# Optimization experiments

Hardware: AMD Instinct MI355X
Metric: run time of the kernel (lower is better)

Reference implementation:

```python
import jax, jax.numpy as jnp
import numpy as np

N_HEADS = 16
D_HEAD = 64
D_MODEL = 1024
N_CTX = 2048
ATTN_SCALE = float(np.sqrt(D_HEAD))
NEG_INF = -jnp.inf


def setup_inputs() -> dict:
    key = jax.random.key(0)
    ks = jax.random.split(key, 6)
    B, S = 2, N_CTX
    q = jax.random.normal(ks[0], (B, S, N_HEADS * D_HEAD), dtype=jnp.float32)
    k = jax.random.normal(ks[1], (B, S, N_HEADS * D_HEAD), dtype=jnp.float32)
    v = jax.random.normal(ks[2], (B, S, N_HEADS * D_HEAD), dtype=jnp.float32)
    residual = jax.random.normal(ks[3], (B, S, D_MODEL), dtype=jnp.float32)
    W_O = jax.random.normal(ks[4], (N_HEADS, D_HEAD, D_MODEL), dtype=jnp.float32) * 0.02
    b_O = jnp.zeros((D_MODEL,), dtype=jnp.float32)
    return {"q": q, "k": k, "v": v, "residual": residual, "W_O": W_O, "b_O": b_O}


def reference(q, k, v, residual, W_O, b_O):
    B, S, _ = q.shape
    # split heads: [..., pos, (h d)] -> [..., pos, h, d]
    qh = q.reshape(B, S, N_HEADS, D_HEAD)
    kh = k.reshape(B, S, N_HEADS, D_HEAD)
    vh = v.reshape(B, S, N_HEADS, D_HEAD)
    # attention scores: [b, h, q_pos, k_pos]
    scores = jnp.einsum('bqhd,bkhd->bhqk', qh, kh) / ATTN_SCALE
    causal = jnp.tril(jnp.ones((S, S), dtype=bool))
    scores = jnp.where(causal, scores, NEG_INF)
    pattern = jax.nn.softmax(scores, axis=-1)
    # z: [b, q_pos, h, d]
    z = jnp.einsum('bkhd,bhqk->bqhd', vh, pattern)
    out = jnp.einsum('bqhd,hdm->bqm', z, W_O) + b_O
    return out, residual
```

## Files before the change

kernel.cpp:

```cpp
#include <hip/hip_runtime.h>

#define BATCH 2
#define SEQ 2048
#define NHEADS 16
#define DHEAD 64
#define DMODEL 1024

typedef __attribute__((ext_vector_type(8))) short bf16x8;
typedef __attribute__((ext_vector_type(4))) float f32x4;

#define QSCALE 0.18033688011112042f

__device__ __forceinline__ unsigned short f2b(float f) {
  union { float f; unsigned u; } a; a.f = f;
  return (unsigned short)((a.u + 0x7fffu + ((a.u >> 16) & 1u)) >> 16);
}

__device__ __forceinline__ unsigned cvt2(float lo, float hi) {
  unsigned r;
  asm("v_cvt_pk_bf16_f32 %0, %1, %2" : "=v"(r) : "v"(lo), "v"(hi));
  return r;
}

#if defined(__has_builtin)
#if __has_builtin(__builtin_amdgcn_exp2f)
#define EXP2(x) __builtin_amdgcn_exp2f(x)
#else
#define EXP2(x) exp2f(x)
#endif
#else
#define EXP2(x) exp2f(x)
#endif

__global__ __launch_bounds__(256) void prep_kernel(
    const float* __restrict__ qg, const float* __restrict__ kg,
    const float* __restrict__ vg, const float* __restrict__ wo,
    const float* __restrict__ residual,
    unsigned short* __restrict__ qb, unsigned short* __restrict__ kb,
    unsigned short* __restrict__ vt, unsigned short* __restrict__ wt,
    float* __restrict__ res_out) {
  __shared__ unsigned short T[64][72];
  const int blk = blockIdx.x;
  const int tid = (int)threadIdx.x;

  if (blk < 4096) {
    const int t = blk * 256 + tid;
    const int d8 = t & 7;
    const int h = (t >> 3) & 15;
    const int q = (t >> 7) & 2047;
    const int b = (t >> 18) & 1;
    const int tensor = (t >> 19) & 1;
    const float* src = (tensor ? kg : qg) +
        ((size_t)(b * SEQ + q) * DMODEL + h * DHEAD + d8 * 8);
    unsigned short* dst = (tensor ? kb : qb) +
        ((size_t)((b * NHEADS + h) * SEQ + q) * DHEAD + d8 * 8);
    const float s = tensor ? 1.0f : QSCALE;
    f32x4 v0 = *(const f32x4*)src;
    f32x4 v1 = *(const f32x4*)(src + 4);
    ushort4 o0, o1;
    o0.x = f2b(v0[0] * s); o0.y = f2b(v0[1] * s);
    o0.z = f2b(v0[2] * s); o0.w = f2b(v0[3] * s);
    o1.x = f2b(v1[0] * s); o1.y = f2b(v1[1] * s);
    o1.z = f2b(v1[2] * s); o1.w = f2b(v1[3] * s);
    *(ushort4*)dst = o0;
    *(ushort4*)(dst + 4) = o1;
  } else if (blk < 5120) {
    const size_t i = ((size_t)(blk - 4096) * 256 + tid) * 16;
    #pragma unroll
    for (int j = 0; j < 4; ++j)
      *(f32x4*)(res_out + i + j * 4) = *(const f32x4*)(residual + i + j * 4);
  } else if (blk < 6144) {
    const int wg = blk - 5120;
    const int kt = wg & 31;
    const int bh = wg >> 5;
    const int row = tid >> 2, quad = tid & 3;
    const int b = bh >> 4, h = bh & 15;
    const float* vp = vg + (size_t)(b * SEQ + kt * 64 + row) * DMODEL + h * DHEAD + quad * 16;
    #pragma unroll
    for (int j = 0; j < 4; ++j) {
      f32x4 x = *(const f32x4*)(vp + j * 4);
      ushort4 o;
      o.x = f2b(x[0]); o.y = f2b(x[1]); o.z = f2b(x[2]); o.w = f2b(x[3]);
      *(ushort4*)&T[row][quad * 16 + j * 4] = o;
    }
    __syncthreads();
    unsigned short* op = vt + ((size_t)bh * DHEAD + row) * SEQ + kt * 64 + quad * 16;
    bf16x8 a, c;
    #pragma unroll
    for (int e = 0; e < 8; ++e) a[e] = (short)T[quad * 16 + e][row];
    #pragma unroll
    for (int e = 0; e < 8; ++e) c[e] = (short)T[quad * 16 + 8 + e][row];
    *(bf16x8*)op = a;
    *(bf16x8*)(op + 8) = c;
  } else {
    const int wg = blk - 6144;
    const int mt = wg & 15;
    const int h = wg >> 4;
    const int row = tid >> 2, quad = tid & 3;
    const float* wp = wo + (size_t)(h * DHEAD + row) * DMODEL + mt * 64 + quad * 16;
    #pragma unroll
    for (int j = 0; j < 4; ++j) {
      f32x4 x = *(const f32x4*)(wp + j * 4);
      ushort4 o;
      o.x = f2b(x[0]); o.y = f2b(x[1]); o.z = f2b(x[2]); o.w = f2b(x[3]);
      *(ushort4*)&T[row][quad * 16 + j * 4] = o;
    }
    __syncthreads();
    unsigned short* op = wt + (size_t)(mt * 64 + row) * DMODEL + h * DHEAD + quad * 16;
    bf16x8 a, c;
    #pragma unroll
    for (int e = 0; e < 8; ++e) a[e] = (short)T[quad * 16 + e][row];
    #pragma unroll
    for (int e = 0; e < 8; ++e) c[e] = (short)T[quad * 16 + 8 + e][row];
    *(bf16x8*)op = a;
    *(bf16x8*)(op + 8) = c;
  }
}

__global__ __launch_bounds__(256) void attn_kernel(
    const unsigned short* __restrict__ qb, const unsigned short* __restrict__ kb,
    const unsigned short* __restrict__ vt, unsigned short* __restrict__ zg) {
  __shared__ unsigned short Kld[64][72];
  __shared__ unsigned short Vtld[64][72];
  __shared__ unsigned short Pld[4][16][72];

  const int wg = (blockIdx.x & 7) * 128 + (blockIdx.x >> 3);
  const int bh = wg >> 5;
  const int qt = (wg & 31) ^ (bh & 31);
  const int tid = (int)threadIdx.x;
  const int w = tid >> 6;
  const int lane = tid & 63;
  const int lg = lane >> 4;
  const int ln = lane & 15;

  bf16x8 qf[2];
  {
    const unsigned short* qp =
        qb + ((size_t)bh * SEQ + qt * 64 + w * 16 + ln) * DHEAD;
    qf[0] = *(const bf16x8*)(qp + lg * 8);
    qf[1] = *(const bf16x8*)(qp + 32 + lg * 8);
  }

  float mrow = -1e30f, lrow = 0.f;
  f32x4 zac[4];
  #pragma unroll
  for (int u = 0; u < 4; ++u) {
    zac[u][0] = 0.f; zac[u][1] = 0.f; zac[u][2] = 0.f; zac[u][3] = 0.f;
  }

  const int row = tid >> 2, quad = tid & 3;
  const int nkt = qt + 1;
  for (int kt = 0; kt < nkt; ++kt) {
    const int k0 = kt * 64;
    {
      const unsigned short* kp = kb + ((size_t)bh * SEQ + k0 + row) * DHEAD + quad * 16;
      const unsigned short* vp = vt + ((size_t)bh * DHEAD + row) * SEQ + k0 + quad * 16;
      *(bf16x8*)&Kld[row][quad * 16]      = *(const bf16x8*)kp;
      *(bf16x8*)&Kld[row][quad * 16 + 8]  = *(const bf16x8*)(kp + 8);
      *(bf16x8*)&Vtld[row][quad * 16]     = *(const bf16x8*)vp;
      *(bf16x8*)&Vtld[row][quad * 16 + 8] = *(const bf16x8*)(vp + 8);
    }
    __syncthreads();

    f32x4 sc[4];
    #pragma unroll
    for (int t = 0; t < 4; ++t) {
      f32x4 s = {0.f, 0.f, 0.f, 0.f};
      #pragma unroll
      for (int c = 0; c < 2; ++c) {
        bf16x8 kf = *(const bf16x8*)&Kld[t * 16 + ln][c * 32 + lg * 8];
        s = __builtin_amdgcn_mfma_f32_16x16x32_bf16(kf, qf[c], s, 0, 0, 0);
      }
      sc[t] = s;
    }

    if (kt == qt) {
      const int qloc = w * 16 + ln;
      #pragma unroll
      for (int t = 0; t < 4; ++t) {
        #pragma unroll
        for (int r = 0; r < 4; ++r) {
          if (t * 16 + lg * 4 + r > qloc) sc[t][r] = -1e30f;
        }
      }
    }

    float mx = sc[0][0];
    #pragma unroll
    for (int t = 0; t < 4; ++t) {
      #pragma unroll
      for (int r = 0; r < 4; ++r) mx = fmaxf(mx, sc[t][r]);
    }
    mx = fmaxf(mx, __shfl_xor(mx, 16, 64));
    mx = fmaxf(mx, __shfl_xor(mx, 32, 64));

    if (!__all(mx <= mrow + 8.f)) {
      const float mnew = fmaxf(mrow, mx);
      const float scl = EXP2(mrow - mnew);
      mrow = mnew;
      lrow *= scl;
      const int sbase = lane & 48;
      const float s0 = __shfl(scl, sbase | (lg * 4 + 0), 64);
      const float s1 = __shfl(scl, sbase | (lg * 4 + 1), 64);
      const float s2 = __shfl(scl, sbase | (lg * 4 + 2), 64);
      const float s3 = __shfl(scl, sbase | (lg * 4 + 3), 64);
      #pragma unroll
      for (int u = 0; u < 4; ++u) {
        zac[u][0] *= s0; zac[u][1] *= s1; zac[u][2] *= s2; zac[u][3] *= s3;
      }
    }

    float rsum = 0.f;
    #pragma unroll
    for (int t = 0; t < 4; ++t) {
      const float p0 = EXP2(sc[t][0] - mrow);
      const float p1 = EXP2(sc[t][1] - mrow);
      const float p2 = EXP2(sc[t][2] - mrow);
      const float p3 = EXP2(sc[t][3] - mrow);
      rsum += (p0 + p1) + (p2 + p3);
      uint2 pk;
      pk.x = cvt2(p0, p1);
      pk.y = cvt2(p2, p3);
      *(uint2*)&Pld[w][ln][t * 16 + lg * 4] = pk;
    }
    rsum += __shfl_xor(rsum, 16, 64);
    rsum += __shfl_xor(rsum, 32, 64);
    lrow += rsum;

    #pragma unroll
    for (int c = 0; c < 2; ++c) {
      bf16x8 pa = *(const bf16x8*)&Pld[w][ln][c * 32 + lg * 8];
      #pragma unroll
      for (int u = 0; u < 4; ++u) {
        bf16x8 vb = *(const bf16x8*)&Vtld[u * 16 + ln][c * 32 + lg * 8];
        zac[u] = __builtin_amdgcn_mfma_f32_16x16x32_bf16(pa, vb, zac[u], 0, 0, 0);
      }
    }
    __syncthreads();
  }

  const int b = bh >> 4, h = bh & 15;
  const int sbase = lane & 48;
  float rl[4];
  #pragma unroll
  for (int i = 0; i < 4; ++i)
    rl[i] = 1.0f / __shfl(lrow, sbase | (lg * 4 + i), 64);
  #pragma unroll
  for (int u = 0; u < 4; ++u) {
    #pragma unroll
    for (int i = 0; i < 4; ++i) {
      const int qrow = qt * 64 + w * 16 + lg * 4 + i;
      zg[((size_t)(b * SEQ + qrow)) * DMODEL + h * DHEAD + u * 16 + ln] =
          f2b(zac[u][i] * rl[i]);
    }
  }
}

__global__ __launch_bounds__(256) void proj_kernel(
    const unsigned short* __restrict__ zb, const unsigned short* __restrict__ wt,
    const float* __restrict__ bo, float* __restrict__ out) {
  __shared__ unsigned short Ald[128][72];
  __shared__ unsigned short Bld[64][72];

  const int m0 = blockIdx.x * 128, n0 = blockIdx.y * 64;
  const int tid = (int)threadIdx.x;
  const int w = tid >> 6, lane = tid & 63, lg = lane >> 4, ln = lane & 15;
  const int wr = w >> 1, wc = w & 1;

  const int arow = tid >> 1, acol = (tid & 1) * 32;
  const int brow = tid >> 2, bcol = (tid & 3) * 16;

  f32x4 acc[4][2];
  #pragma unroll
  for (int a = 0; a < 4; ++a)
    #pragma unroll
    for (int bj = 0; bj < 2; ++bj) {
      acc[a][bj][0] = 0.f; acc[a][bj][1] = 0.f;
      acc[a][bj][2] = 0.f; acc[a][bj][3] = 0.f;
    }

  bf16x8 ra[4], rb[2];
  {
    const unsigned short* ap = zb + (size_t)(m0 + arow) * DMODEL + acol;
    const unsigned short* bp = wt + (size_t)(n0 + brow) * DMODEL + bcol;
    #pragma unroll
    for (int j = 0; j < 4; ++j) ra[j] = *(const bf16x8*)(ap + j * 8);
    rb[0] = *(const bf16x8*)(bp);
    rb[1] = *(const bf16x8*)(bp + 8);
  }

  for (int ks = 0; ks < DMODEL / 64; ++ks) {
    __syncthreads();
    #pragma unroll
    for (int j = 0; j < 4; ++j) *(bf16x8*)&Ald[arow][acol + j * 8] = ra[j];
    *(bf16x8*)&Bld[brow][bcol]     = rb[0];
    *(bf16x8*)&Bld[brow][bcol + 8] = rb[1];
    __syncthreads();

    if (ks + 1 < DMODEL / 64) {
      const int k0 = (ks + 1) * 64;
      const unsigned short* ap = zb + (size_t)(m0 + arow) * DMODEL + k0 + acol;
      const unsigned short* bp = wt + (size_t)(n0 + brow) * DMODEL + k0 + bcol;
      #pragma unroll
      for (int j = 0; j < 4; ++j) ra[j] = *(const bf16x8*)(ap + j * 8);
      rb[0] = *(const bf16x8*)(bp);
      rb[1] = *(const bf16x8*)(bp + 8);
    }

    #pragma unroll
    for (int c = 0; c < 2; ++c) {
      bf16x8 bf[2];
      #pragma unroll
      for (int bj = 0; bj < 2; ++bj)
        bf[bj] = *(const bf16x8*)&Bld[wc * 32 + bj * 16 + ln][c * 32 + lg * 8];
      #pragma unroll
      for (int a = 0; a < 4; ++a) {
        bf16x8 af = *(const bf16x8*)&Ald[wr * 64 + a * 16 + ln][c * 32 + lg * 8];
        #pragma unroll
        for (int bj = 0; bj < 2; ++bj)
          acc[a][bj] = __builtin_amdgcn_mfma_f32_16x16x32_bf16(af, bf[bj], acc[a][bj], 0, 0, 0);
      }
    }
  }

  #pragma unroll
  for (int a = 0; a < 4; ++a)
    #pragma unroll
    for (int bj = 0; bj < 2; ++bj) {
      const int nc = n0 + wc * 32 + bj * 16 + ln;
      const float bias = bo[nc];
      #pragma unroll
      for (int i = 0; i < 4; ++i) {
        const int mr = m0 + wr * 64 + a * 16 + lg * 4 + i;
        out[(size_t)mr * DMODEL + nc] = acc[a][bj][i] + bias;
      }
    }
}

extern "C" void kernel_launch(void* const* d_in, const int* in_sizes, int n_in,
                              void* d_out, int out_size, void* d_ws, size_t ws_size,
                              hipStream_t stream) {
  const float* q        = (const float*)d_in[0];
  const float* k        = (const float*)d_in[1];
  const float* v        = (const float*)d_in[2];
  const float* residual = (const float*)d_in[3];
  const float* wo       = (const float*)d_in[4];
  const float* bo       = (const float*)d_in[5];
  float* out = (float*)d_out;

  const size_t QN = (size_t)BATCH * NHEADS * SEQ * DHEAD;
  unsigned short* qbuf = (unsigned short*)d_ws;
  unsigned short* kbuf = qbuf + QN;
  unsigned short* vtb  = qbuf + 2 * QN;
  unsigned short* wtb  = qbuf + 3 * QN;
  unsigned short* zb   = qbuf + 3 * QN + (size_t)DMODEL * DMODEL;

  prep_kernel<<<dim3(6400), 256, 0, stream>>>(
      q, k, v, wo, residual, qbuf, kbuf, vtb, wtb,
      out + (size_t)BATCH * SEQ * DMODEL);
  attn_kernel<<<dim3(BATCH * NHEADS * (SEQ / 64)), 256, 0, stream>>>(qbuf, kbuf, vtb, zb);
  proj_kernel<<<dim3(BATCH * SEQ / 128, DMODEL / 64), 256, 0, stream>>>(zb, wtb, bo, out);
}
```

Measured before the change: 202.1 us.

## Pair complementary causal q-tiles per block, prefetch K/V, deepen proj K-step

Each attention workgroup now handles two query tiles (ip and 31-ip), so every block does the same amount of causal work and shares each staged K/V tile between both. The grid is halved. The next K/V tile is prefetched into registers while the current one is computed, and the LDS padding changes from 72 to 68. The projection GEMM now stages 128-wide K slices, which halves its barrier count but raises register and LDS use. The exp2 builtin is replaced with exp2f, and the 68-column padding risks misaligned 16-byte LDS accesses and bank conflicts.

```diff
diff --git a/kernel.cpp b/kernel.cpp
--- a/kernel.cpp
+++ b/kernel.cpp
@@ -22,15 +22,7 @@
   return r;
 }
 
-#if defined(__has_builtin)
-#if __has_builtin(__builtin_amdgcn_exp2f)
-#define EXP2(x) __builtin_amdgcn_exp2f(x)
-#else
 #define EXP2(x) exp2f(x)
-#endif
-#else
-#define EXP2(x) exp2f(x)
-#endif
 
 __global__ __launch_bounds__(256) void prep_kernel(
     const float* __restrict__ qg, const float* __restrict__ kg,
@@ -120,48 +112,46 @@
 __global__ __launch_bounds__(256) void attn_kernel(
     const unsigned short* __restrict__ qb, const unsigned short* __restrict__ kb,
     const unsigned short* __restrict__ vt, unsigned short* __restrict__ zg) {
-  __shared__ unsigned short Kld[64][72];
-  __shared__ unsigned short Vtld[64][72];
-  __shared__ unsigned short Pld[4][16][72];
-
-  const int wg = (blockIdx.x & 7) * 128 + (blockIdx.x >> 3);
-  const int bh = wg >> 5;
-  const int qt = (wg & 31) ^ (bh & 31);
+  __shared__ unsigned short Kld[64][68];
+  __shared__ unsigned short Vtld[64][68];
+  __shared__ unsigned short Pld[4][16][68];
+
+  const int wg = (blockIdx.x & 7) * 64 + (blockIdx.x >> 3);
+  const int bh = wg >> 4;
+  const int ip = wg & 15;
+  const int qtA = ip, qtB = 31 - ip;
   const int tid = (int)threadIdx.x;
   const int w = tid >> 6;
   const int lane = tid & 63;
   const int lg = lane >> 4;
   const int ln = lane & 15;
 
-  bf16x8 qf[2];
+  bf16x8 qfA[2], qfB[2];
   {
-    const unsigned short* qp =
-        qb + ((size_t)bh * SEQ + qt * 64 + w * 16 + ln) * DHEAD;
-    qf[0] = *(const bf16x8*)(qp + lg * 8);
-    qf[1] = *(const bf16x8*)(qp + 32 + lg * 8);
-  }
-
-  float mrow = -1e30f, lrow = 0.f;
-  f32x4 zac[4];
+    const unsigned short* qpA =
+        qb + ((size_t)bh * SEQ + qtA * 64 + w * 16 + ln) * DHEAD;
+    const unsigned short* qpB =
+        qb + ((size_t)bh * SEQ + qtB * 64 + w * 16 + ln) * DHEAD;
+    qfA[0] = *(const bf16x8*)(qpA + lg * 8);
+    qfA[1] = *(const bf16x8*)(qpA + 32 + lg * 8);
+    qfB[0] = *(const bf16x8*)(qpB + lg * 8);
+    qfB[1] = *(const bf16x8*)(qpB + 32 + lg * 8);
+  }
+
+  float mA = -1e30f, lA = 0.f, mB = -1e30f, lB = 0.f;
+  f32x4 zacA[4], zacB[4];
   #pragma unroll
   for (int u = 0; u < 4; ++u) {
-    zac[u][0] = 0.f; zac[u][1] = 0.f; zac[u][2] = 0.f; zac[u][3] = 0.f;
+    zacA[u][0] = 0.f; zacA[u][1] = 0.f; zacA[u][2] = 0.f; zacA[u][3] = 0.f;
+    zacB[u][0] = 0.f; zacB[u][1] = 0.f; zacB[u][2] = 0.f; zacB[u][3] = 0.f;
   }
 
   const int row = tid >> 2, quad = tid & 3;
-  const int nkt = qt + 1;
-  for (int kt = 0; kt < nkt; ++kt) {
-    const int k0 = kt * 64;
-    {
-      const unsigned short* kp = kb + ((size_t)bh * SEQ + k0 + row) * DHEAD + quad * 16;
-      const unsigned short* vp = vt + ((size_t)bh * DHEAD + row) * SEQ + k0 + quad * 16;
-      *(bf16x8*)&Kld[row][quad * 16]      = *(const bf16x8*)kp;
-      *(bf16x8*)&Kld[row][quad * 16 + 8]  = *(const bf16x8*)(kp + 8);
-      *(bf16x8*)&Vtld[row][quad * 16]     = *(const bf16x8*)vp;
-      *(bf16x8*)&Vtld[row][quad * 16 + 8] = *(const bf16x8*)(vp + 8);
-    }
-    __syncthreads();
-
+  const unsigned short* kbase = kb + (size_t)bh * SEQ * DHEAD;
+  const unsigned short* vbase = vt + (size_t)bh * DHEAD * SEQ;
+
+  auto compute = [&](const bf16x8* qf, float& mrow, float& lrow, f32x4* zac,
+                     bool diag) {
     f32x4 sc[4];
     #pragma unroll
     for (int t = 0; t < 4; ++t) {
@@ -173,24 +163,19 @@
       }
       sc[t] = s;
     }
-
-    if (kt == qt) {
+    if (diag) {
       const int qloc = w * 16 + ln;
       #pragma unroll
-      for (int t = 0; t < 4; ++t) {
+      for (int t = 0; t < 4; ++t)
         #pragma unroll
-        for (int r = 0; r < 4; ++r) {
+        for (int r = 0; r < 4; ++r)
           if (t * 16 + lg * 4 + r > qloc) sc[t][r] = -1e30f;
-        }
-      }
-    }
-
+    }
     float mx = sc[0][0];
     #pragma unroll
-    for (int t = 0; t < 4; ++t) {
+    for (int t = 0; t < 4; ++t)
       #pragma unroll
       for (int r = 0; r < 4; ++r) mx = fmaxf(mx, sc[t][r]);
-    }
     mx = fmaxf(mx, __shfl_xor(mx, 16, 64));
     mx = fmaxf(mx, __shfl_xor(mx, 32, 64));
 
@@ -236,39 +221,68 @@
         zac[u] = __builtin_amdgcn_mfma_f32_16x16x32_bf16(pa, vb, zac[u], 0, 0, 0);
       }
     }
+  };
+
+  const int nkt = qtB + 1;
+  bf16x8 rk0, rk1, rv0, rv1;
+  {
+    const unsigned short* kp = kbase + (size_t)row * DHEAD + quad * 16;
+    const unsigned short* vp = vbase + (size_t)row * SEQ + quad * 16;
+    rk0 = *(const bf16x8*)kp;  rk1 = *(const bf16x8*)(kp + 8);
+    rv0 = *(const bf16x8*)vp;  rv1 = *(const bf16x8*)(vp + 8);
+  }
+
+  for (int kt = 0; kt < nkt; ++kt) {
+    if (kt) __syncthreads();
+    *(bf16x8*)&Kld[row][quad * 16]      = rk0;
+    *(bf16x8*)&Kld[row][quad * 16 + 8]  = rk1;
+    *(bf16x8*)&Vtld[row][quad * 16]     = rv0;
+    *(bf16x8*)&Vtld[row][quad * 16 + 8] = rv1;
     __syncthreads();
+    if (kt + 1 < nkt) {
+      const int k0 = (kt + 1) * 64;
+      const unsigned short* kp = kbase + (size_t)(k0 + row) * DHEAD + quad * 16;
+      const unsigned short* vp = vbase + (size_t)row * SEQ + k0 + quad * 16;
+      rk0 = *(const bf16x8*)kp;  rk1 = *(const bf16x8*)(kp + 8);
+      rv0 = *(const bf16x8*)vp;  rv1 = *(const bf16x8*)(vp + 8);
+    }
+    if (kt <= qtA) compute(qfA, mA, lA, zacA, kt == qtA);
+    compute(qfB, mB, lB, zacB, kt == qtB);
   }
 
   const int b = bh >> 4, h = bh & 15;
   const int sbase = lane & 48;
-  float rl[4];
-  #pragma unroll
-  for (int i = 0; i < 4; ++i)
-    rl[i] = 1.0f / __shfl(lrow, sbase | (lg * 4 + i), 64);
-  #pragma unroll
-  for (int u = 0; u < 4; ++u) {
-    #pragma unroll
-    for (int i = 0; i < 4; ++i) {
-      const int qrow = qt * 64 + w * 16 + lg * 4 + i;
-      zg[((size_t)(b * SEQ + qrow)) * DMODEL + h * DHEAD + u * 16 + ln] =
-          f2b(zac[u][i] * rl[i]);
-    }
-  }
+  auto epi = [&](int qt, float lrow, const f32x4* zac) {
+    float rl[4];
+    #pragma unroll
+    for (int i = 0; i < 4; ++i)
+      rl[i] = 1.0f / __shfl(lrow, sbase | (lg * 4 + i), 64);
+    #pragma unroll
+    for (int u = 0; u < 4; ++u)
+      #pragma unroll
+      for (int i = 0; i < 4; ++i) {
+        const int qrow = qt * 64 + w * 16 + lg * 4 + i;
+        zg[((size_t)(b * SEQ + qrow)) * DMODEL + h * DHEAD + u * 16 + ln] =
+            f2b(zac[u][i] * rl[i]);
+      }
+  };
+  epi(qtA, lA, zacA);
+  epi(qtB, lB, zacB);
 }
 
 __global__ __launch_bounds__(256) void proj_kernel(
     const unsigned short* __restrict__ zb, const unsigned short* __restrict__ wt,
     const float* __restrict__ bo, float* __restrict__ out) {
-  __shared__ unsigned short Ald[128][72];
-  __shared__ unsigned short Bld[64][72];
+  __shared__ unsigned short Ald[128][136];
+  __shared__ unsigned short Bld[64][136];
 
   const int m0 = blockIdx.x * 128, n0 = blockIdx.y * 64;
   const int tid = (int)threadIdx.x;
   const int w = tid >> 6, lane = tid & 63, lg = lane >> 4, ln = lane & 15;
   const int wr = w >> 1, wc = w & 1;
 
-  const int arow = tid >> 1, acol = (tid & 1) * 32;
-  const int brow = tid >> 2, bcol = (tid & 3) * 16;
+  const int arow = tid >> 1, acol = (tid & 1) * 64;
+  const int brow = tid >> 2, bcol = (tid & 3) * 32;
 
   f32x4 acc[4][2];
   #pragma unroll
@@ -279,36 +293,36 @@
       acc[a][bj][2] = 0.f; acc[a][bj][3] = 0.f;
     }
 
-  bf16x8 ra[4], rb[2];
+  bf16x8 ra[8], rb[4];
   {
     const unsigned short* ap = zb + (size_t)(m0 + arow) * DMODEL + acol;
     const unsigned short* bp = wt + (size_t)(n0 + brow) * DMODEL + bcol;
     #pragma unroll
-    for (int j = 0; j < 4; ++j) ra[j] = *(const bf16x8*)(ap + j * 8);
-    rb[0] = *(const bf16x8*)(bp);
-    rb[1] = *(const bf16x8*)(bp + 8);
-  }
-
-  for (int ks = 0; ks < DMODEL / 64; ++ks) {
+    for (int j = 0; j < 8; ++j) ra[j] = *(const bf16x8*)(ap + j * 8);
+    #pragma unroll
+    for (int j = 0; j < 4; ++j) rb[j] = *(const bf16x8*)(bp + j * 8);
+  }
+
+  for (int ks = 0; ks < DMODEL / 128; ++ks) {
+    if (ks) __syncthreads();
+    #pragma unroll
+    for (int j = 0; j < 8; ++j) *(bf16x8*)&Ald[arow][acol + j * 8] = ra[j];
+    #pragma unroll
+    for (int j = 0; j < 4; ++j) *(bf16x8*)&Bld[brow][bcol + j * 8] = rb[j];
     __syncthreads();
-    #pragma unroll
-    for (int j = 0; j < 4; ++j) *(bf16x8*)&Ald[arow][acol + j * 8] = ra[j];
-    *(bf16x8*)&Bld[brow][bcol]     = rb[0];
-    *(bf16x8*)&Bld[brow][bcol + 8] = rb[1];
-    __syncthreads();
-
-    if (ks + 1 < DMODEL / 64) {
-      const int k0 = (ks + 1) * 64;
+
+    if (ks + 1 < DMODEL / 128) {
+      const int k0 = (ks + 1) * 128;
       const unsigned short* ap = zb + (size_t)(m0 + arow) * DMODEL + k0 + acol;
       const unsigned short* bp = wt + (size_t)(n0 + brow) * DMODEL + k0 + bcol;
       #pragma unroll
-      for (int j = 0; j < 4; ++j) ra[j] = *(const bf16x8*)(ap + j * 8);
-      rb[0] = *(const bf16x8*)(bp);
-      rb[1] = *(const bf16x8*)(bp + 8);
-    }
-
-    #pragma unroll
-    for (int c = 0; c < 2; ++c) {
+      for (int j = 0; j < 8; ++j) ra[j] = *(const bf16x8*)(ap + j * 8);
+      #pragma unroll
+      for (int j = 0; j < 4; ++j) rb[j] = *(const bf16x8*)(bp + j * 8);
+    }
+
+    #pragma unroll
+    for (int c = 0; c < 4; ++c) {
       bf16x8 bf[2];
       #pragma unroll
       for (int bj = 0; bj < 2; ++bj)
@@ -358,6 +372,6 @@
   prep_kernel<<<dim3(6400), 256, 0, stream>>>(
       q, k, v, wo, residual, qbuf, kbuf, vtb, wtb,
       out + (size_t)BATCH * SEQ * DMODEL);
-  attn_kernel<<<dim3(BATCH * NHEADS * (SEQ / 64)), 256, 0, stream>>>(qbuf, kbuf, vtb, zb);
+  attn_kernel<<<dim3(512), 256, 0, stream>>>(qbuf, kbuf, vtb, zb);
   proj_kernel<<<dim3(BATCH * SEQ / 128, DMODEL / 64), 256, 0, stream>>>(zb, wtb, bo, out);
 }
```

Result: faster. 196.2 us (-2.9%).
